# Optimization experiments

Measured on AMD Instinct MI355X. Metric: run time of the kernel, lower is better.

## Reference

```python
import jax, jax.numpy as jnp
import numpy as np

EPS = 1e-12  # tf.math.l2_normalize epsilon

def _l2norm3(v):
    # 3 * l2_normalize(v, axis=-1), tf semantics: v / sqrt(max(sum(v^2), eps))
    sq = jnp.sum(v * v, axis=-1, keepdims=True)
    return 3.0 * v * jax.lax.rsqrt(jnp.maximum(sq, EPS))

def setup_inputs() -> dict:
    key = jax.random.key(0)
    k1, k2 = jax.random.split(key)
    B, C, D = 4096, 16384, 128
    inputs = jax.random.normal(k1, (B, D), dtype=jnp.float32)
    kernel = jax.random.normal(k2, (C, D), dtype=jnp.float32)
    return {"inputs": inputs, "kernel": kernel}

def reference(inputs, kernel):
    x = _l2norm3(inputs)        # [B, D]
    p = _l2norm3(kernel)        # [C, D]
    xs = jnp.sum(x * x, axis=-1, keepdims=True)          # [B, 1]
    ps = jnp.sum(p * p, axis=-1)                          # [C]
    cross = jnp.einsum('bd,cd->bc', x, p)                 # [B, C]
    return xs + ps[None, :] - 2.0 * cross                 # [B, C]
```

## Files before the change

kernel.cpp:

```cpp
#include <hip/hip_runtime.h>

typedef __attribute__((ext_vector_type(8))) short short8;
typedef __attribute__((ext_vector_type(4))) float f32x4;

__device__ __forceinline__ unsigned short f32_to_bf16(float f) {
    union { float f; unsigned int u; } c; c.f = f;
    unsigned int u = c.u;
    unsigned int r = (u + 0x7fffu + ((u >> 16) & 1u)) >> 16;
    return (unsigned short)r;
}

__global__ void norm_kernel(const float* __restrict__ inA,
                            const float* __restrict__ inB,
                            int nA,
                            unsigned short* __restrict__ xout,
                            float* __restrict__ sout) {
    const int row  = blockIdx.x * 4 + (threadIdx.x >> 6);
    const int lane = threadIdx.x & 63;
    const float* src = (row < nA) ? (inA + (size_t)row * 128)
                                  : (inB + (size_t)(row - nA) * 128);
    const float2 v = ((const float2*)src)[lane];
    float s = fmaf(v.x, v.x, v.y * v.y);
#pragma unroll
    for (int off = 32; off; off >>= 1) s += __shfl_xor(s, off, 64);
    const float r  = rsqrtf(fmaxf(s, 1e-12f));
    const float sc = 3.0f * r;
    ushort2 o;
    o.x = f32_to_bf16(v.x * sc);
    o.y = f32_to_bf16(v.y * sc);
    ((ushort2*)(xout + (size_t)row * 128))[lane] = o;
    if (lane == 0) sout[row] = 9.0f * s * (r * r);
}

__global__ __launch_bounds__(256, 2) void gemm_kernel(
    const unsigned short* __restrict__ A,
    const unsigned short* __restrict__ B,
    const float* __restrict__ xs,
    const float* __restrict__ ps,
    float* __restrict__ out,
    int Ncols)
{
    __shared__ unsigned short sA[128 * 128];
    __shared__ unsigned short sB[128 * 128];

    const int tid  = threadIdx.x;
    const int lane = tid & 63;
    const int wave = tid >> 6;
    const int bm   = blockIdx.y;
    const int bn   = blockIdx.x;

    const int wm   = (wave >> 1) * 64;
    const int wn   = (wave & 1) * 64;
    const int l15  = lane & 15;
    const int quad = lane >> 4;

    float xsr[4];
    float psr[16];
#pragma unroll
    for (int mt = 0; mt < 4; ++mt)
        xsr[mt] = xs[bm * 128 + wm + mt * 16 + l15];
#pragma unroll
    for (int nt = 0; nt < 4; ++nt)
#pragma unroll
        for (int r = 0; r < 4; ++r)
            psr[nt * 4 + r] = ps[bn * 128 + wn + nt * 16 + quad * 4 + r];

    {
        const char* gA = (const char*)(A + (size_t)bm * 128 * 128);
        const char* gB = (const char*)(B + (size_t)bn * 128 * 128);
#pragma unroll
        for (int it = 0; it < 8; ++it) {
            const int cid = it * 256 + wave * 64 + lane;
            const int m   = cid >> 4;
            const int jj  = cid & 15;
            const int gj  = jj ^ (m & 7);
            const int gbyte = m * 256 + gj * 16;
            const int lbyte = cid * 16;
            __builtin_amdgcn_global_load_lds(
                (const __attribute__((address_space(1))) void*)(gA + gbyte),
                (__attribute__((address_space(3))) void*)((char*)sA + lbyte),
                16, 0, 0);
            __builtin_amdgcn_global_load_lds(
                (const __attribute__((address_space(1))) void*)(gB + gbyte),
                (__attribute__((address_space(3))) void*)((char*)sB + lbyte),
                16, 0, 0);
        }
    }
    __syncthreads();

    f32x4 acc[4][4];
#pragma unroll
    for (int i = 0; i < 4; ++i)
#pragma unroll
        for (int j = 0; j < 4; ++j)
            acc[i][j] = (f32x4){0.f, 0.f, 0.f, 0.f};

#pragma unroll
    for (int kk = 0; kk < 4; ++kk) {
        short8 af[4], bfv[4];
#pragma unroll
        for (int mt = 0; mt < 4; ++mt) {
            const int m  = wm + mt * 16 + l15;
            const int jj = (kk * 4 + quad) ^ (m & 7);
            af[mt] = *(const short8*)&sA[m * 128 + jj * 8];
        }
#pragma unroll
        for (int nt = 0; nt < 4; ++nt) {
            const int n  = wn + nt * 16 + l15;
            const int jj = (kk * 4 + quad) ^ (n & 7);
            bfv[nt] = *(const short8*)&sB[n * 128 + jj * 8];
        }
#pragma unroll
        for (int mt = 0; mt < 4; ++mt)
#pragma unroll
            for (int nt = 0; nt < 4; ++nt)
                acc[mt][nt] = __builtin_amdgcn_mfma_f32_16x16x32_bf16(
                    bfv[nt], af[mt], acc[mt][nt], 0, 0, 0);
    }

    const size_t stride = (size_t)Ncols;
#pragma unroll
    for (int mt = 0; mt < 4; ++mt) {
        const int grow = bm * 128 + wm + mt * 16 + l15;
        float* orow = out + (size_t)grow * stride;
#pragma unroll
        for (int nt = 0; nt < 4; ++nt) {
            const int gcol = bn * 128 + wn + nt * 16 + quad * 4;
            f32x4 v;
#pragma unroll
            for (int r = 0; r < 4; ++r)
                v[r] = fmaf(-2.0f, acc[mt][nt][r], xsr[mt] + psr[nt * 4 + r]);
            *(f32x4*)(orow + gcol) = v;
        }
    }
}

extern "C" void kernel_launch(void* const* d_in, const int* in_sizes, int n_in,
                              void* d_out, int out_size, void* d_ws, size_t ws_size,
                              hipStream_t stream) {
    const float* inputs = (const float*)d_in[0];
    const float* kern   = (const float*)d_in[1];
    float* out          = (float*)d_out;

    const int D = 128;
    const int B = in_sizes[0] / D;
    const int C = in_sizes[1] / D;

    char* ws = (char*)d_ws;
    unsigned short* xA = (unsigned short*)ws;
    unsigned short* pB = (unsigned short*)(ws + (size_t)B * D * 2);
    float* xs = (float*)(ws + (size_t)(B + C) * D * 2);
    float* ps = xs + B;

    norm_kernel<<<(B + C) / 4, 256, 0, stream>>>(inputs, kern, B, xA, xs);

    dim3 grid(C / 128, B / 128);
    gemm_kernel<<<grid, 256, 0, stream>>>(xA, pB, xs, ps, out, C);
}
```

Baseline: 281.5 us.

## Load MFMA operands directly from global memory, dropping LDS staging

Removes the shared-memory staging of the A and B tiles and the block barrier, so each wave reads its bf16 MFMA fragments straight from global memory (served by L1/L2). Without LDS use, occupancy can rise, and the launch bound is raised to 3 blocks per CU. Output stores become nontemporal to avoid polluting caches with the large write-only result. The trade-off is that operands shared between waves are no longer reused through LDS, which adds global and cache traffic and exposes load latency.

```diff
diff --git a/kernel.cpp b/kernel.cpp
--- a/kernel.cpp
+++ b/kernel.cpp
@@ -32,7 +32,7 @@
     if (lane == 0) sout[row] = 9.0f * s * (r * r);
 }
 
-__global__ __launch_bounds__(256, 2) void gemm_kernel(
+__global__ __launch_bounds__(256, 3) void gemm_kernel(
     const unsigned short* __restrict__ A,
     const unsigned short* __restrict__ B,
     const float* __restrict__ xs,
@@ -40,9 +40,6 @@
     float* __restrict__ out,
     int Ncols)
 {
-    __shared__ unsigned short sA[128 * 128];
-    __shared__ unsigned short sB[128 * 128];
-
     const int tid  = threadIdx.x;
     const int lane = tid & 63;
     const int wave = tid >> 6;
@@ -65,28 +62,9 @@
         for (int r = 0; r < 4; ++r)
             psr[nt * 4 + r] = ps[bn * 128 + wn + nt * 16 + quad * 4 + r];
 
-    {
-        const char* gA = (const char*)(A + (size_t)bm * 128 * 128);
-        const char* gB = (const char*)(B + (size_t)bn * 128 * 128);
-#pragma unroll
-        for (int it = 0; it < 8; ++it) {
-            const int cid = it * 256 + wave * 64 + lane;
-            const int m   = cid >> 4;
-            const int jj  = cid & 15;
-            const int gj  = jj ^ (m & 7);
-            const int gbyte = m * 256 + gj * 16;
-            const int lbyte = cid * 16;
-            __builtin_amdgcn_global_load_lds(
-                (const __attribute__((address_space(1))) void*)(gA + gbyte),
-                (__attribute__((address_space(3))) void*)((char*)sA + lbyte),
-                16, 0, 0);
-            __builtin_amdgcn_global_load_lds(
-                (const __attribute__((address_space(1))) void*)(gB + gbyte),
-                (__attribute__((address_space(3))) void*)((char*)sB + lbyte),
-                16, 0, 0);
-        }
-    }
-    __syncthreads();
+    const unsigned short* Ab = A + (size_t)(bm * 128 + wm) * 128;
+    const unsigned short* Bb = B + (size_t)(bn * 128 + wn) * 128;
+    const int loff = l15 * 128 + quad * 8;
 
     f32x4 acc[4][4];
 #pragma unroll
@@ -99,16 +77,9 @@
     for (int kk = 0; kk < 4; ++kk) {
         short8 af[4], bfv[4];
 #pragma unroll
-        for (int mt = 0; mt < 4; ++mt) {
-            const int m  = wm + mt * 16 + l15;
-            const int jj = (kk * 4 + quad) ^ (m & 7);
-            af[mt] = *(const short8*)&sA[m * 128 + jj * 8];
-        }
-#pragma unroll
-        for (int nt = 0; nt < 4; ++nt) {
-            const int n  = wn + nt * 16 + l15;
-            const int jj = (kk * 4 + quad) ^ (n & 7);
-            bfv[nt] = *(const short8*)&sB[n * 128 + jj * 8];
+        for (int t = 0; t < 4; ++t) {
+            af[t]  = *(const short8*)(Ab + t * 16 * 128 + kk * 32 + loff);
+            bfv[t] = *(const short8*)(Bb + t * 16 * 128 + kk * 32 + loff);
         }
 #pragma unroll
         for (int mt = 0; mt < 4; ++mt)
@@ -130,7 +101,7 @@
 #pragma unroll
             for (int r = 0; r < 4; ++r)
                 v[r] = fmaf(-2.0f, acc[mt][nt][r], xsr[mt] + psr[nt * 4 + r]);
-            *(f32x4*)(orow + gcol) = v;
+            __builtin_nontemporal_store(v, (f32x4*)(orow + gcol));
         }
     }
 }
```

Result: slower. 312.7 us (+11.1%).
